# Performance work log

Hardware: AMD Instinct MI355X
Metric: run time of the kernel (lower is better)

## Reference

```python
import jax, jax.numpy as jnp
import numpy as np

B, N, M, C, K = 2, 8192, 4096, 64, 16
HID = 256
EPS_BN = 1e-5


def setup_inputs() -> dict:
    key = jax.random.key(0)
    ks = jax.random.split(key, 16)
    def rn(i, shape, scale=1.0):
        return jax.random.normal(ks[i], shape, jnp.float32) * scale
    return {
        "pcl": rn(0, (B, M, 3)),
        "pcl_noise": rn(1, (B, N, 3)),
        "feature": rn(2, (B, M, C)),
        # MLP_CONV (2d 1x1): 6 -> 256 (BN+ReLU) -> C
        "w2a": rn(3, (HID, 6), 0.3), "b2a": rn(4, (HID,), 0.1),
        "g2a": 1.0 + rn(5, (HID,), 0.1), "bt2a": rn(6, (HID,), 0.1),
        "w2b": rn(7, (C, HID), 0.1), "b2b": rn(8, (C,), 0.1),
        # MLP_CONV_1d: 3C -> C (BN+ReLU) -> C
        "w1a": rn(9, (C, 3 * C), 0.1), "b1a": rn(10, (C,), 0.1),
        "g1a": 1.0 + rn(11, (C,), 0.1), "bt1a": rn(12, (C,), 0.1),
        "w1b": rn(13, (C, C), 0.1), "b1b": rn(14, (C,), 0.1),
    }


def _sqdist(x, y):  # [B,n,3],[B,m,3] -> [B,n,m]
    return (jnp.sum(x * x, -1, keepdims=True)
            - 2.0 * jnp.einsum('bnc,bmc->bnm', x, y)
            + jnp.sum(y * y, -1)[:, None, :])


def _gather(x, idx):  # x [B,M,D], idx [B,...] -> [B,...,D]
    return jax.vmap(lambda xb, ib: xb[ib])(x, idx)


def _bn(h, g, b):  # inference BatchNorm: running mean 0, var 1
    return h * (g / jnp.sqrt(1.0 + EPS_BN)) + b


def reference(pcl, pcl_noise, feature, w2a, b2a, g2a, bt2a, w2b, b2b,
              w1a, b1a, g1a, bt1a, w1b, b1b):
    # nearest clean point for each noisy point (knn_points K=1)
    close_idx = jnp.argmin(_sqdist(pcl_noise, pcl), axis=-1)          # [B,N]
    close_point = _gather(pcl, close_idx)                             # [B,N,3]
    # K nearest neighbors of close_point within pcl (dil_knn, d=1)
    _, idx = jax.lax.top_k(-_sqdist(close_point, pcl), K)             # [B,N,K]
    knn_points = _gather(pcl, idx)[:, :, 1:, :]                       # [B,N,K-1,3]
    knn_feat = _gather(feature, idx)[:, :, 1:, :]                     # [B,N,K-1,C]
    close_feat = _gather(feature, close_idx)                          # [B,N,C]

    delta = knn_points - pcl_noise[:, :, None, :]                     # [B,N,K-1,3]
    dst = jnp.linalg.norm(delta, axis=-1)                             # [B,N,K-1]
    e = jnp.exp(-10.0 * dst)
    weight = e / (jnp.sum(e, -1, keepdims=True) + 1e-7)               # [B,N,K-1]

    cp = jnp.broadcast_to(close_point[:, :, None, :], delta.shape)
    delta_points = jnp.concatenate([delta, cp], axis=-1)              # [B,N,K-1,6]

    # MLP_CONV2 (1x1 convs over channel dim)
    h = jnp.einsum('bnkc,oc->bnko', delta_points, w2a) + b2a
    h = jax.nn.relu(_bn(h, g2a, bt2a))
    pf = jnp.einsum('bnkc,oc->bnko', h, w2b) + b2b                    # [B,N,K-1,C]

    point_feature = jnp.einsum('bnk,bnkc->bnc', weight, pf)           # [B,N,C]
    co_feature = jnp.einsum('bnk,bnkc->bnc', weight, knn_feat)        # [B,N,C]
    df = jnp.concatenate([close_feat, co_feature, point_feature], -1)  # [B,N,3C]

    # MLP_CONV_1d
    h1 = jnp.einsum('bnc,oc->bno', df, w1a) + b1a
    h1 = jax.nn.relu(_bn(h1, g1a, bt1a))
    return jnp.einsum('bnc,oc->bno', h1, w1b) + b1b                   # [B,N,C]
```

## Files before the change

### kernel.cpp

```cpp
#include <hip/hip_runtime.h>
#include <float.h>

typedef unsigned short u16;
typedef unsigned int u32;
typedef unsigned char u8;

typedef float f32x4 __attribute__((ext_vector_type(4)));
typedef short bh8   __attribute__((ext_vector_type(8)));

__device__ __forceinline__ float bf(u16 u) { return __uint_as_float(((u32)u) << 16); }
__device__ __forceinline__ u16 f2bf(float v) {
    u32 x = __float_as_uint(v);
    u32 r = x + 0x7fffu + ((x >> 16) & 1u);
    return (u16)(r >> 16);
}
__device__ __forceinline__ int detect_f32(const void* probe) {
    const u16* u = (const u16*)probe;
    u16 v = u[(threadIdx.x & 63) * 2];
    int e = (int)((v >> 7) & 0xFF);
    int moderate = (e >= 100) && (e <= 140);
    return __popcll(__ballot(moderate)) < 48;
}
__device__ __forceinline__ float ldv(int f32, const void* p, int i) {
    return f32 ? ((const float*)p)[i] : bf(((const u16*)p)[i]);
}
__device__ __forceinline__ float dot3(float x0, float x1, float x2,
                                      float y0, float y1, float y2) {
    return __fmaf_rn(x2, y2, __fmaf_rn(x1, y1, __fmul_rn(x0, y0)));
}
__device__ __forceinline__ u32 mkey32(float d) {
    u32 f = __float_as_uint(d);
    return f ^ (u32)((((int)f) >> 31) | 0x80000000);
}
__device__ __forceinline__ bh8 ldb(const void* p) { return *(const bh8*)p; }
__device__ __forceinline__ f32x4 mfma16(bh8 a, bh8 b, f32x4 c) {
    return __builtin_amdgcn_mfma_f32_16x16x32_bf16(a, b, c, 0, 0, 0);
}

__global__ __launch_bounds__(256) void k_pre(const void* __restrict__ probe,
                                             const void* __restrict__ w2b,
                                             const void* __restrict__ w1a,
                                             const void* __restrict__ w1b,
                                             u32* __restrict__ canonb,
                                             const void* __restrict__ pcl,
                                             float4* __restrict__ pcl4) {
    int f32 = detect_f32(probe);
    int bx = blockIdx.x, t = threadIdx.x;
    if (bx < 64) {
        int ix = bx * 256 + t;
        const void* src; int j;
        if (ix < 8192)       { src = w2b; j = ix; }
        else if (ix < 14336) { src = w1a; j = ix - 8192; }
        else                 { src = w1b; j = ix - 14336; }
        u32 out;
        if (f32) {
            const float* f = (const float*)src;
            out = ((u32)f2bf(f[2*j+1]) << 16) | (u32)f2bf(f[2*j]);
        } else {
            const u16* su = (const u16*)src;
            out = ((u32)su[2*j+1] << 16) | (u32)su[2*j];
        }
        canonb[ix] = out;
    } else {
        int i = (bx - 64) * 256 + t;
        float x = ldv(f32, pcl, i*3+0), y = ldv(f32, pcl, i*3+1), z = ldv(f32, pcl, i*3+2);
        float s = __fadd_rn(__fadd_rn(__fmul_rn(x,x), __fmul_rn(y,y)), __fmul_rn(z,z));
        pcl4[i] = make_float4(x, y, z, s);
    }
}

__global__ __launch_bounds__(256) void k_sel(const float4* __restrict__ pcl4,
                                             const void* __restrict__ noise,
                                             u16* __restrict__ cidx,
                                             u16* __restrict__ knn) {
    __shared__ __align__(16) char arena[16384];
    int bx = blockIdx.x;
    int r9 = bx % 9, c9 = bx / 9;
    int t = threadIdx.x, lane = t & 63, wv = t >> 6;

    if (r9 == 0) {
        float4* tile = (float4*)arena;
        int f32 = detect_f32(noise);
        int g = t >> 4, s = t & 15;
        int q = c9 * 16 + g;
        int b = q >> 13;
        const float4* src = pcl4 + ((size_t)b << 12);
        float x0 = ldv(f32, noise, q*3+0), x1 = ldv(f32, noise, q*3+1), x2 = ldv(f32, noise, q*3+2);
        float sx = __fadd_rn(__fadd_rn(__fmul_rn(x0,x0), __fmul_rn(x1,x1)), __fmul_rn(x2,x2));
        float bd = FLT_MAX; int bi = 0;
        for (int ch = 0; ch < 4; ++ch) {
            __syncthreads();
#pragma unroll
            for (int i = 0; i < 4; ++i) { int ix = t + (i << 8); tile[ix] = src[(ch << 10) + ix]; }
            __syncthreads();
            for (int j = 0; j < 64; ++j) {
                int cl = (j << 4) + s;
                float4 p = tile[cl];
                float dot = dot3(x0, x1, x2, p.x, p.y, p.z);
                float d = __fadd_rn(__fsub_rn(sx, __fmul_rn(2.0f, dot)), p.w);
                int c = (ch << 10) + cl;
                if (d < bd) { bd = d; bi = c; }
            }
        }
#pragma unroll
        for (int m = 8; m >= 1; m >>= 1) {
            float od = __shfl_xor(bd, m);
            int   oi = __shfl_xor(bi, m);
            if (od < bd || (od == bd && oi < bi)) { bd = od; bi = oi; }
        }
        if (s == 0) cidx[q] = (u16)(bi & 4095);
        return;
    }

    u8*  bins = (u8*)arena;
    u32* hist = (u32*)(arena + 4096);
    u32* skey = (u32*)(arena + 5120);
    u16* sidx = (u16*)(arena + 6144);
    float* rmn = (float*)(arena + 6656);
    float* rmx = (float*)(arena + 6672);
    u32* scnt = (u32*)(arena + 6688);
    int* ibst = (int*)(arena + 6692);

    int q = c9 * 8 + (r9 - 1);
    int b = q >> 12;
    const float4* src = pcl4 + ((size_t)b << 12);
    float4 Q = src[q & 4095];
    float x0 = Q.x, x1 = Q.y, x2 = Q.z, sx = Q.w;
    hist[t] = 0;
    if (t == 0) *scnt = 0;
    {
        float4 p = src[t << 4];
        float dot = dot3(x0, x1, x2, p.x, p.y, p.z);
        float d = __fadd_rn(__fsub_rn(sx, __fmul_rn(2.0f, dot)), p.w);
        float mn = d, mx = d;
#pragma unroll
        for (int m = 32; m >= 1; m >>= 1) {
            mn = fminf(mn, __shfl_xor(mn, m));
            mx = fmaxf(mx, __shfl_xor(mx, m));
        }
        if (lane == 0) { rmn[wv] = mn; rmx[wv] = mx; }
    }
    __syncthreads();
    float dmn = fminf(fminf(rmn[0], rmn[1]), fminf(rmn[2], rmn[3]));
    float dmx = fmaxf(fmaxf(rmx[0], rmx[1]), fmaxf(rmx[2], rmx[3]));
    float sc = 1024.0f / fmaxf(dmx - dmn, 1e-20f);
#pragma unroll 4
    for (int j = 0; j < 16; ++j) {
        int cin = (j << 8) + t;
        float4 p = src[cin];
        float dot = dot3(x0, x1, x2, p.x, p.y, p.z);
        float d = __fadd_rn(__fsub_rn(sx, __fmul_rn(2.0f, dot)), p.w);
        float fb = fminf(fmaxf((d - dmn) * sc, 0.0f), 255.0f);
        int bn = (int)fb;
        bins[cin] = (u8)bn;
        if (bn < 255) atomicAdd(&hist[bn], 1u);
    }
    __syncthreads();
    if (t < 64) {
        u32 c0 = hist[4*lane], c1 = hist[4*lane+1];
        u32 c2 = hist[4*lane+2], c3 = hist[4*lane+3];
        u32 loc = c0 + c1 + c2 + c3;
        u32 x = loc;
#pragma unroll
        for (int off = 1; off < 64; off <<= 1) { u32 v = __shfl_up(x, off); if (lane >= off) x += v; }
        u32 excl = x - loc;
        int cand = 999;
        if (excl + c0 >= 16u) cand = 4*lane;
        else if (excl + c0 + c1 >= 16u) cand = 4*lane + 1;
        else if (excl + c0 + c1 + c2 >= 16u) cand = 4*lane + 2;
        else if (excl + loc >= 16u) cand = 4*lane + 3;
#pragma unroll
        for (int m = 32; m >= 1; m >>= 1) cand = min(cand, __shfl_xor(cand, m));
        if (lane == 0) *ibst = cand;
    }
    __syncthreads();
    int bstar = *ibst;
#pragma unroll
    for (int j = 0; j < 16; ++j) {
        int cin = (j << 8) + t;
        if ((int)bins[cin] <= bstar) {
            u32 pos = atomicAdd(scnt, 1u);
            if (pos < 256u) {
                float4 p = src[cin];
                float dot = dot3(x0, x1, x2, p.x, p.y, p.z);
                float d = __fadd_rn(__fsub_rn(sx, __fmul_rn(2.0f, dot)), p.w);
                skey[pos] = mkey32(d);
                sidx[pos] = (u16)cin;
            }
        }
    }
    __syncthreads();
    u32 n = *scnt;
    if (n <= 256u) {
        for (u32 e = (u32)t; e < n; e += 256u) {
            u32 k = skey[e]; u32 i = (u32)sidx[e];
            int rank = 0;
            for (u32 j = 0; j < n; ++j) {
                u32 kj = skey[j]; u32 ij = (u32)sidx[j];
                rank += (kj < k) || (kj == k && ij < i);
            }
            if (rank < 16) knn[((size_t)q << 4) + rank] = (u16)i;
        }
    } else if (t < 64) {
        u32 k0=~0u,k1=~0u,k2=~0u,k3=~0u,k4=~0u,k5=~0u,k6=~0u,k7=~0u,
            k8=~0u,k9=~0u,k10=~0u,k11=~0u,k12=~0u,k13=~0u,k14=~0u,k15=~0u;
        u32 i0r=0,i1r=0,i2r=0,i3r=0,i4r=0,i5r=0,i6r=0,i7r=0,
            i8r=0,i9r=0,i10r=0,i11r=0,i12r=0,i13r=0,i14r=0,i15r=0;
        for (int j = 0; j < 64; ++j) {
            int cin = (j << 6) + lane;
            float4 p = src[cin];
            float dot = dot3(x0, x1, x2, p.x, p.y, p.z);
            float d = __fadd_rn(__fsub_rn(sx, __fmul_rn(2.0f, dot)), p.w);
            u32 v = mkey32(d); u32 vi = (u32)cin;
            if (v < k15) {
                { u32 c_=(v<k0); u32 nk=c_?v:k0; u32 nv=c_?k0:v; u32 ni=c_?vi:i0r; u32 nj=c_?i0r:vi; k0=nk;i0r=ni;v=nv;vi=nj; }
                { u32 c_=(v<k1); u32 nk=c_?v:k1; u32 nv=c_?k1:v; u32 ni=c_?vi:i1r; u32 nj=c_?i1r:vi; k1=nk;i1r=ni;v=nv;vi=nj; }
                { u32 c_=(v<k2); u32 nk=c_?v:k2; u32 nv=c_?k2:v; u32 ni=c_?vi:i2r; u32 nj=c_?i2r:vi; k2=nk;i2r=ni;v=nv;vi=nj; }
                { u32 c_=(v<k3); u32 nk=c_?v:k3; u32 nv=c_?k3:v; u32 ni=c_?vi:i3r; u32 nj=c_?i3r:vi; k3=nk;i3r=ni;v=nv;vi=nj; }
                { u32 c_=(v<k4); u32 nk=c_?v:k4; u32 nv=c_?k4:v; u32 ni=c_?vi:i4r; u32 nj=c_?i4r:vi; k4=nk;i4r=ni;v=nv;vi=nj; }
                { u32 c_=(v<k5); u32 nk=c_?v:k5; u32 nv=c_?k5:v; u32 ni=c_?vi:i5r; u32 nj=c_?i5r:vi; k5=nk;i5r=ni;v=nv;vi=nj; }
                { u32 c_=(v<k6); u32 nk=c_?v:k6; u32 nv=c_?k6:v; u32 ni=c_?vi:i6r; u32 nj=c_?i6r:vi; k6=nk;i6r=ni;v=nv;vi=nj; }
                { u32 c_=(v<k7); u32 nk=c_?v:k7; u32 nv=c_?k7:v; u32 ni=c_?vi:i7r; u32 nj=c_?i7r:vi; k7=nk;i7r=ni;v=nv;vi=nj; }
                { u32 c_=(v<k8); u32 nk=c_?v:k8; u32 nv=c_?k8:v; u32 ni=c_?vi:i8r; u32 nj=c_?i8r:vi; k8=nk;i8r=ni;v=nv;vi=nj; }
                { u32 c_=(v<k9); u32 nk=c_?v:k9; u32 nv=c_?k9:v; u32 ni=c_?vi:i9r; u32 nj=c_?i9r:vi; k9=nk;i9r=ni;v=nv;vi=nj; }
                { u32 c_=(v<k10); u32 nk=c_?v:k10; u32 nv=c_?k10:v; u32 ni=c_?vi:i10r; u32 nj=c_?i10r:vi; k10=nk;i10r=ni;v=nv;vi=nj; }
                { u32 c_=(v<k11); u32 nk=c_?v:k11; u32 nv=c_?k11:v; u32 ni=c_?vi:i11r; u32 nj=c_?i11r:vi; k11=nk;i11r=ni;v=nv;vi=nj; }
                { u32 c_=(v<k12); u32 nk=c_?v:k12; u32 nv=c_?k12:v; u32 ni=c_?vi:i12r; u32 nj=c_?i12r:vi; k12=nk;i12r=ni;v=nv;vi=nj; }
                { u32 c_=(v<k13); u32 nk=c_?v:k13; u32 nv=c_?k13:v; u32 ni=c_?vi:i13r; u32 nj=c_?i13r:vi; k13=nk;i13r=ni;v=nv;vi=nj; }
                { u32 c_=(v<k14); u32 nk=c_?v:k14; u32 nv=c_?k14:v; u32 ni=c_?vi:i14r; u32 nj=c_?i14r:vi; k14=nk;i14r=ni;v=nv;vi=nj; }
                { u32 c_=(v<k15); u32 nk=c_?v:k15; u32 nv=c_?k15:v; u32 ni=c_?vi:i15r; u32 nj=c_?i15r:vi; k15=nk;i15r=ni;v=nv;vi=nj; }
            }
        }
        u32 myres = 0;
        for (int o = 0; o < 16; ++o) {
            u32 bk = k0, bi2 = i0r;
#pragma unroll
            for (int m = 32; m >= 1; m >>= 1) {
                u32 ok = __shfl_xor(bk, m), oi = __shfl_xor(bi2, m);
                if (ok < bk || (ok == bk && oi < bi2)) { bk = ok; bi2 = oi; }
            }
            if (lane == o) myres = bi2;
            if (k0 == bk && i0r == bi2) {
                k0=k1; i0r=i1r; k1=k2; i1r=i2r; k2=k3; i2r=i3r; k3=k4; i3r=i4r;
                k4=k5; i4r=i5r; k5=k6; i5r=i6r; k6=k7; i6r=i7r; k7=k8; i7r=i8r;
                k8=k9; i8r=i9r; k9=k10; i9r=i10r; k10=k11; i10r=i11r; k11=k12; i11r=i12r;
                k12=k13; i12r=i13r; k13=k14; i13r=i14r; k14=k15; i14r=i15r;
                k15=~0u; i15r=0xFFFFu;
            }
        }
        if (lane < 16) knn[((size_t)q << 4) + lane] = (u16)myres;
    }
}

__global__ __launch_bounds__(256) void k_tail(const float4* __restrict__ pcl4,
                                              const void* __restrict__ noise,
                                              const void* __restrict__ feat,
                                              const u16* __restrict__ cidx,
                                              const u16* __restrict__ knn,
                                              const void* __restrict__ w2a,
                                              const void* __restrict__ b2a,
                                              const void* __restrict__ g2a,
                                              const void* __restrict__ bt2a,
                                              const u32* __restrict__ canonb,
                                              const void* __restrict__ b2b,
                                              const void* __restrict__ b1a,
                                              const void* __restrict__ g1a,
                                              const void* __restrict__ bt1a,
                                              const void* __restrict__ b1b,
                                              void* __restrict__ outp) {
    __shared__ __align__(16) char arena[39744];
    char* dpb_hi = arena;
    char* dpb_lo = arena + 4352;
    char* wbt    = arena + 8704;
    char* wsbp   = arena + 9984;
    u16*  jbuf   = (u16*)(arena + 10048);
    char* hbm_   = arena + 10560;
    char* dfm    = arena + 27200;
    char* h1m    = arena;

    int f32 = detect_f32(noise);
    int t = threadIdx.x, lane = t & 63, wv = t >> 6;
    int g = lane >> 4, l15 = lane & 15;
    int qbb = blockIdx.x * 16;
    int o_lane = wv * 16 + l15;
    const float rbn = 1.0f / sqrtf(1.0f + 1e-5f);
    const char* cb = (const char*)canonb;
    const f32x4 zero4 = {0.f, 0.f, 0.f, 0.f};

    float of2r[4];
    bh8 wH[4];
#pragma unroll
    for (int j = 0; j < 4; ++j) {
        int oh = wv*64 + j*16 + l15;
        float sc = ldv(f32, g2a, oh) * rbn;
        of2r[j] = ldv(f32, b2a, oh) * sc + ldv(f32, bt2a, oh);
        bh8 wz = (bh8){0,0,0,0,0,0,0,0};
        if (g < 3) {
#pragma unroll
            for (int c = 0; c < 6; ++c) {
                float wval = ldv(f32, w2a, oh*6 + c) * sc;
                u16 h = f2bf(wval);
                u16 e = (g == 2) ? f2bf(wval - bf(h)) : h;
                wz[c] = (short)e;
            }
        }
        wH[j] = wz;
    }
    float s1o  = ldv(f32, g1a, o_lane) * rbn;
    float o1o  = ldv(f32, b1a, o_lane) * s1o + ldv(f32, bt1a, o_lane);
    float b2bo = ldv(f32, b2b, o_lane);
    float b1fo = ldv(f32, b1b, o_lane);

    {
        int s = lane & 15;
        int ql = wv*4 + (lane >> 4);
        int q = qbb + ql;
        int pbase = (q >> 13) << 12;
        int ci = ((int)cidx[q]) & 4095;
        float4 cp = pcl4[pbase + ci];
        float x0 = ldv(f32, noise, q*3+0), x1 = ldv(f32, noise, q*3+1), x2 = ldv(f32, noise, q*3+2);
        float e = 0.0f;
        if (s >= 1) {
            int jk = ((int)knn[(size_t)(pbase + ci) * 16 + s]) & 4095;
            float4 p = pcl4[pbase + jk];
            float d0 = p.x - x0, d1 = p.y - x1, d2 = p.z - x2;
            float dst = sqrtf(__fadd_rn(__fadd_rn(__fmul_rn(d0,d0), __fmul_rn(d1,d1)), __fmul_rn(d2,d2)));
            e = expf(-10.0f * dst);
            float v6[6] = {d0, d1, d2, cp.x, cp.y, cp.z};
            bh8 HW = (bh8){0,0,0,0,0,0,0,0};
            bh8 LW = (bh8){0,0,0,0,0,0,0,0};
#pragma unroll
            for (int c = 0; c < 6; ++c) {
                u16 hh = f2bf(v6[c]);
                u16 ll = f2bf(v6[c] - bf(hh));
                HW[c] = (short)hh;
                LW[c] = (short)ll;
            }
            *(bh8*)(dpb_hi + (ql*17 + s)*16) = HW;
            *(bh8*)(dpb_lo + (ql*17 + s)*16) = LW;
            jbuf[ql*16 + s] = (u16)jk;
        }
        float es = e;
#pragma unroll
        for (int m = 8; m >= 1; m >>= 1) es += __shfl_xor(es, m, 16);
        float den = es + 1e-7f;
        if (s >= 1) *(float*)(wbt + s*80 + ql*4) = e / den;
        if (s == 0) *(float*)(wsbp + ql*4) = es / den;
    }
    __syncthreads();

#pragma unroll
    for (int qq = 0; qq < 4; ++qq) {
        int qloc = wv*4 + qq;
        int q = qbb + qloc;
        int pbase = (q >> 13) << 12;
        int ci = ((int)cidx[q]) & 4095;
        size_t fcb = ((size_t)(pbase + ci)) << 6;
        float c0, c1 = 0.0f;
        if (f32) {
            const float* ff = (const float*)feat;
            c0 = ff[fcb + lane];
#pragma unroll
            for (int k = 1; k < 16; ++k) {
                float wk = *(const float*)(wbt + k*80 + qloc*4);
                c1 += wk * ff[(((size_t)(pbase + (int)jbuf[qloc*16 + k])) << 6) + lane];
            }
        } else {
            const u16* fb = (const u16*)feat;
            c0 = bf(fb[fcb + lane]);
#pragma unroll
            for (int k = 1; k < 16; ++k) {
                float wk = *(const float*)(wbt + k*80 + qloc*4);
                c1 += wk * bf(fb[(((size_t)(pbase + (int)jbuf[qloc*16 + k])) << 6) + lane]);
            }
        }
        char* dr = dfm + qloc*784;
        u16 h0 = f2bf(c0); u16 l0 = f2bf(c0 - bf(h0));
        u16 h1v = f2bf(c1); u16 l1v = f2bf(c1 - bf(h1v));
        *(u16*)(dr + (size_t)lane*2)         = h0;
        *(u16*)(dr + (size_t)(192+lane)*2)   = l0;
        *(u16*)(dr + (size_t)(64+lane)*2)    = h1v;
        *(u16*)(dr + (size_t)(256+lane)*2)   = l1v;
    }

    {
        f32x4 hba[4];
#pragma unroll
        for (int j = 0; j < 4; ++j) hba[j] = zero4;
#pragma unroll 2
        for (int k = 1; k < 16; ++k) {
            bh8 af;
            if (g < 3) {
                const char* base = (g == 1) ? dpb_lo : dpb_hi;
                af = ldb(base + (l15*17 + k)*16);
            } else {
                af = (bh8){0,0,0,0,0,0,0,0};
            }
            f32x4 wk4 = *(const f32x4*)(wbt + k*80 + g*16);
#pragma unroll
            for (int j = 0; j < 4; ++j) {
                f32x4 d = mfma16(af, wH[j], zero4);
#pragma unroll
                for (int r = 0; r < 4; ++r)
                    hba[j][r] += wk4[r] * fmaxf(d[r] + of2r[j], 0.0f);
            }
        }
#pragma unroll
        for (int j = 0; j < 4; ++j)
#pragma unroll
            for (int r = 0; r < 4; ++r) {
                int q = g*4 + r;
                int o = wv*64 + j*16 + l15;
                float x = hba[j][r];
                u16 h = f2bf(x); u16 l = f2bf(x - bf(h));
                *(u16*)(hbm_ + q*1040 + (size_t)o*2)       = h;
                *(u16*)(hbm_ + q*1040 + 512 + (size_t)o*2) = l;
            }
    }
    __syncthreads();

    {
        f32x4 acA = zero4, acB = zero4;
#pragma unroll 2
        for (int ks = 0; ks < 8; ++ks) {
            bh8 bw = ldb(cb + (size_t)o_lane*512 + ks*64 + g*16);
            bh8 aH = ldb(hbm_ + l15*1040 + ks*64 + g*16);
            bh8 aL = ldb(hbm_ + l15*1040 + 512 + ks*64 + g*16);
            acA = mfma16(aH, bw, acA);
            acB = mfma16(aL, bw, acB);
        }
        f32x4 wsb4 = *(const f32x4*)(wsbp + g*16);
#pragma unroll
        for (int r = 0; r < 4; ++r) {
            int q = g*4 + r;
            float pf = acA[r] + acB[r] + b2bo * wsb4[r];
            u16 h = f2bf(pf); u16 l = f2bf(pf - bf(h));
            *(u16*)(dfm + q*784 + (size_t)(128 + o_lane)*2) = h;
            *(u16*)(dfm + q*784 + (size_t)(320 + o_lane)*2) = l;
        }
    }
    __syncthreads();

    {
        f32x4 acA = zero4, acB = zero4;
#pragma unroll 2
        for (int ks = 0; ks < 6; ++ks) {
            bh8 bw = ldb(cb + 32768 + (size_t)o_lane*384 + ks*64 + g*16);
            bh8 aH = ldb(dfm + l15*784 + ks*64 + g*16);
            bh8 aL = ldb(dfm + l15*784 + 384 + ks*64 + g*16);
            acA = mfma16(aH, bw, acA);
            acB = mfma16(aL, bw, acB);
        }
#pragma unroll
        for (int r = 0; r < 4; ++r) {
            int q = g*4 + r;
            float z = (acA[r] + acB[r]) * s1o + o1o;
            z = fmaxf(z, 0.0f);
            u16 h = f2bf(z); u16 l = f2bf(z - bf(h));
            *(u16*)(h1m + q*272 + (size_t)o_lane*2)       = h;
            *(u16*)(h1m + q*272 + 128 + (size_t)o_lane*2) = l;
        }
    }
    __syncthreads();

    {
        bh8 bw0 = ldb(cb + 57344 + (size_t)o_lane*128 + g*16);
        bh8 bw1 = ldb(cb + 57344 + (size_t)o_lane*128 + 64 + g*16);
        f32x4 ac = zero4;
        { bh8 a = ldb(h1m + l15*272 +   0 + g*16); ac = mfma16(a, bw0, ac); }
        { bh8 a = ldb(h1m + l15*272 +  64 + g*16); ac = mfma16(a, bw1, ac); }
        { bh8 a = ldb(h1m + l15*272 + 128 + g*16); ac = mfma16(a, bw0, ac); }
        { bh8 a = ldb(h1m + l15*272 + 192 + g*16); ac = mfma16(a, bw1, ac); }
#pragma unroll
        for (int r = 0; r < 4; ++r) {
            int q = g*4 + r;
            float ov = ac[r] + b1fo;
            size_t ob = ((size_t)(qbb + q) << 6) + o_lane;
            if (f32) ((float*)outp)[ob] = ov;
            else     ((u16*)outp)[ob]   = f2bf(ov);
        }
    }
}

extern "C" void kernel_launch(void* const* d_in, const int* in_sizes, int n_in,
                              void* d_out, int out_size, void* d_ws, size_t ws_size,
                              hipStream_t stream) {
    const void* pcl   = d_in[0];
    const void* noise = d_in[1];
    const void* feat  = d_in[2];
    const void* w2a   = d_in[3];
    const void* b2a   = d_in[4];
    const void* g2a   = d_in[5];
    const void* bt2a  = d_in[6];
    const void* w2b   = d_in[7];
    const void* b2b   = d_in[8];
    const void* w1a   = d_in[9];
    const void* b1a   = d_in[10];
    const void* g1a   = d_in[11];
    const void* bt1a  = d_in[12];
    const void* w1b   = d_in[13];
    const void* b1b   = d_in[14];

    char* ws = (char*)d_ws;
    float4* pcl4 = (float4*)ws;
    u16* cidx = (u16*)(ws + 131072);
    u16* knn  = (u16*)(ws + 163840);
    u32* canonb = (u32*)(ws + 425984);

    k_pre  <<<96,   256, 0, stream>>>(noise, w2b, w1a, w1b, canonb, pcl, pcl4);
    k_sel  <<<9216, 256, 0, stream>>>(pcl4, noise, cidx, knn);
    k_tail <<<1024, 256, 0, stream>>>(pcl4, noise, feat, cidx, knn,
                                      w2a, b2a, g2a, bt2a, canonb, b2b,
                                      b1a, g1a, bt1a, b1b, d_out);
}
```

Baseline: 213.3 us.

## Process two kNN queries per block in k_sel to share point-cloud loads

```diff
diff --git a/kernel.cpp b/kernel.cpp
--- a/kernel.cpp
+++ b/kernel.cpp
@@ -28,6 +28,10 @@
                                       float y0, float y1, float y2) {
     return __fmaf_rn(x2, y2, __fmaf_rn(x1, y1, __fmul_rn(x0, y0)));
 }
+__device__ __forceinline__ float qdist(float x0, float x1, float x2, float sx, float4 p) {
+    float dot = dot3(x0, x1, x2, p.x, p.y, p.z);
+    return __fadd_rn(__fsub_rn(sx, __fmul_rn(2.0f, dot)), p.w);
+}
 __device__ __forceinline__ u32 mkey32(float d) {
     u32 f = __float_as_uint(d);
     return f ^ (u32)((((int)f) >> 31) | 0x80000000);
@@ -35,6 +39,56 @@
 __device__ __forceinline__ bh8 ldb(const void* p) { return *(const bh8*)p; }
 __device__ __forceinline__ f32x4 mfma16(bh8 a, bh8 b, f32x4 c) {
     return __builtin_amdgcn_mfma_f32_16x16x32_bf16(a, b, c, 0, 0, 0);
+}
+
+__device__ __forceinline__ void knn_fallback(const float4* __restrict__ src,
+                                             float x0, float x1, float x2, float sx,
+                                             int q, u16* __restrict__ knn, int lane) {
+    u32 k0=~0u,k1=~0u,k2=~0u,k3=~0u,k4=~0u,k5=~0u,k6=~0u,k7=~0u,
+        k8=~0u,k9=~0u,k10=~0u,k11=~0u,k12=~0u,k13=~0u,k14=~0u,k15=~0u;
+    u32 i0r=0,i1r=0,i2r=0,i3r=0,i4r=0,i5r=0,i6r=0,i7r=0,
+        i8r=0,i9r=0,i10r=0,i11r=0,i12r=0,i13r=0,i14r=0,i15r=0;
+    for (int j = 0; j < 64; ++j) {
+        int cin = (j << 6) + lane;
+        float d = qdist(x0, x1, x2, sx, src[cin]);
+        u32 v = mkey32(d); u32 vi = (u32)cin;
+        if (v < k15) {
+            { u32 c_=(v<k0); u32 nk=c_?v:k0; u32 nv=c_?k0:v; u32 ni=c_?vi:i0r; u32 nj=c_?i0r:vi; k0=nk;i0r=ni;v=nv;vi=nj; }
+            { u32 c_=(v<k1); u32 nk=c_?v:k1; u32 nv=c_?k1:v; u32 ni=c_?vi:i1r; u32 nj=c_?i1r:vi; k1=nk;i1r=ni;v=nv;vi=nj; }
+            { u32 c_=(v<k2); u32 nk=c_?v:k2; u32 nv=c_?k2:v; u32 ni=c_?vi:i2r; u32 nj=c_?i2r:vi; k2=nk;i2r=ni;v=nv;vi=nj; }
+            { u32 c_=(v<k3); u32 nk=c_?v:k3; u32 nv=c_?k3:v; u32 ni=c_?vi:i3r; u32 nj=c_?i3r:vi; k3=nk;i3r=ni;v=nv;vi=nj; }
+            { u32 c_=(v<k4); u32 nk=c_?v:k4; u32 nv=c_?k4:v; u32 ni=c_?vi:i4r; u32 nj=c_?i4r:vi; k4=nk;i4r=ni;v=nv;vi=nj; }
+            { u32 c_=(v<k5); u32 nk=c_?v:k5; u32 nv=c_?k5:v; u32 ni=c_?vi:i5r; u32 nj=c_?i5r:vi; k5=nk;i5r=ni;v=nv;vi=nj; }
+            { u32 c_=(v<k6); u32 nk=c_?v:k6; u32 nv=c_?k6:v; u32 ni=c_?vi:i6r; u32 nj=c_?i6r:vi; k6=nk;i6r=ni;v=nv;vi=nj; }
+            { u32 c_=(v<k7); u32 nk=c_?v:k7; u32 nv=c_?k7:v; u32 ni=c_?vi:i7r; u32 nj=c_?i7r:vi; k7=nk;i7r=ni;v=nv;vi=nj; }
+            { u32 c_=(v<k8); u32 nk=c_?v:k8; u32 nv=c_?k8:v; u32 ni=c_?vi:i8r; u32 nj=c_?i8r:vi; k8=nk;i8r=ni;v=nv;vi=nj; }
+            { u32 c_=(v<k9); u32 nk=c_?v:k9; u32 nv=c_?k9:v; u32 ni=c_?vi:i9r; u32 nj=c_?i9r:vi; k9=nk;i9r=ni;v=nv;vi=nj; }
+            { u32 c_=(v<k10); u32 nk=c_?v:k10; u32 nv=c_?k10:v; u32 ni=c_?vi:i10r; u32 nj=c_?i10r:vi; k10=nk;i10r=ni;v=nv;vi=nj; }
+            { u32 c_=(v<k11); u32 nk=c_?v:k11; u32 nv=c_?k11:v; u32 ni=c_?vi:i11r; u32 nj=c_?i11r:vi; k11=nk;i11r=ni;v=nv;vi=nj; }
+            { u32 c_=(v<k12); u32 nk=c_?v:k12; u32 nv=c_?k12:v; u32 ni=c_?vi:i12r; u32 nj=c_?i12r:vi; k12=nk;i12r=ni;v=nv;vi=nj; }
+            { u32 c_=(v<k13); u32 nk=c_?v:k13; u32 nv=c_?k13:v; u32 ni=c_?vi:i13r; u32 nj=c_?i13r:vi; k13=nk;i13r=ni;v=nv;vi=nj; }
+            { u32 c_=(v<k14); u32 nk=c_?v:k14; u32 nv=c_?k14:v; u32 ni=c_?vi:i14r; u32 nj=c_?i14r:vi; k14=nk;i14r=ni;v=nv;vi=nj; }
+            { u32 c_=(v<k15); u32 nk=c_?v:k15; u32 nv=c_?k15:v; u32 ni=c_?vi:i15r; u32 nj=c_?i15r:vi; k15=nk;i15r=ni;v=nv;vi=nj; }
+        }
+    }
+    u32 myres = 0;
+    for (int o = 0; o < 16; ++o) {
+        u32 bk = k0, bi2 = i0r;
+#pragma unroll
+        for (int m = 32; m >= 1; m >>= 1) {
+            u32 ok = __shfl_xor(bk, m), oi = __shfl_xor(bi2, m);
+            if (ok < bk || (ok == bk && oi < bi2)) { bk = ok; bi2 = oi; }
+        }
+        if (lane == o) myres = bi2;
+        if (k0 == bk && i0r == bi2) {
+            k0=k1; i0r=i1r; k1=k2; i1r=i2r; k2=k3; i2r=i3r; k3=k4; i3r=i4r;
+            k4=k5; i4r=i5r; k5=k6; i5r=i6r; k6=k7; i6r=i7r; k7=k8; i7r=i8r;
+            k8=k9; i8r=i9r; k9=k10; i9r=i10r; k10=k11; i10r=i11r; k11=k12; i11r=i12r;
+            k12=k13; i12r=i13r; k13=k14; i13r=i14r; k14=k15; i14r=i15r;
+            k15=~0u; i15r=0xFFFFu;
+        }
+    }
+    if (lane < 16) knn[((size_t)q << 4) + lane] = (u16)myres;
 }
 
 __global__ __launch_bounds__(256) void k_pre(const void* __restrict__ probe,
@@ -73,32 +127,31 @@
                                              const void* __restrict__ noise,
                                              u16* __restrict__ cidx,
                                              u16* __restrict__ knn) {
-    __shared__ __align__(16) char arena[16384];
+    __shared__ __align__(16) char arena[32768];
     int bx = blockIdx.x;
-    int r9 = bx % 9, c9 = bx / 9;
+    int r5 = bx % 5, c5 = bx / 5;
     int t = threadIdx.x, lane = t & 63, wv = t >> 6;
 
-    if (r9 == 0) {
+    if (r5 == 0) {
         float4* tile = (float4*)arena;
         int f32 = detect_f32(noise);
         int g = t >> 4, s = t & 15;
-        int q = c9 * 16 + g;
+        int q = c5 * 16 + g;
         int b = q >> 13;
         const float4* src = pcl4 + ((size_t)b << 12);
         float x0 = ldv(f32, noise, q*3+0), x1 = ldv(f32, noise, q*3+1), x2 = ldv(f32, noise, q*3+2);
         float sx = __fadd_rn(__fadd_rn(__fmul_rn(x0,x0), __fmul_rn(x1,x1)), __fmul_rn(x2,x2));
         float bd = FLT_MAX; int bi = 0;
-        for (int ch = 0; ch < 4; ++ch) {
+        for (int ch = 0; ch < 2; ++ch) {
             __syncthreads();
 #pragma unroll
-            for (int i = 0; i < 4; ++i) { int ix = t + (i << 8); tile[ix] = src[(ch << 10) + ix]; }
+            for (int i = 0; i < 8; ++i) { int ix = t + (i << 8); tile[ix] = src[(ch << 11) + ix]; }
             __syncthreads();
-            for (int j = 0; j < 64; ++j) {
+            for (int j = 0; j < 128; ++j) {
                 int cl = (j << 4) + s;
                 float4 p = tile[cl];
-                float dot = dot3(x0, x1, x2, p.x, p.y, p.z);
-                float d = __fadd_rn(__fsub_rn(sx, __fmul_rn(2.0f, dot)), p.w);
-                int c = (ch << 10) + cl;
+                float d = qdist(x0, x1, x2, sx, p);
+                int c = (ch << 11) + cl;
                 if (d < bd) { bd = d; bi = c; }
             }
         }
@@ -112,53 +165,72 @@
         return;
     }
 
-    u8*  bins = (u8*)arena;
-    u32* hist = (u32*)(arena + 4096);
-    u32* skey = (u32*)(arena + 5120);
-    u16* sidx = (u16*)(arena + 6144);
-    float* rmn = (float*)(arena + 6656);
-    float* rmx = (float*)(arena + 6672);
-    u32* scnt = (u32*)(arena + 6688);
-    int* ibst = (int*)(arena + 6692);
-
-    int q = c9 * 8 + (r9 - 1);
-    int b = q >> 12;
+    u8*  bins0 = (u8*)arena;
+    u8*  bins1 = (u8*)(arena + 4096);
+    u32* hist0 = (u32*)(arena + 8192);
+    u32* hist1 = (u32*)(arena + 9216);
+    u32* skey0 = (u32*)(arena + 10240);
+    u32* skey1 = (u32*)(arena + 11264);
+    u16* sidx0 = (u16*)(arena + 12288);
+    u16* sidx1 = (u16*)(arena + 12800);
+    float* rmn0 = (float*)(arena + 13312);
+    float* rmx0 = (float*)(arena + 13328);
+    float* rmn1 = (float*)(arena + 13344);
+    float* rmx1 = (float*)(arena + 13360);
+    u32* scnt0 = (u32*)(arena + 13376);
+    u32* scnt1 = (u32*)(arena + 13380);
+    int* ibst0 = (int*)(arena + 13384);
+    int* ibst1 = (int*)(arena + 13388);
+
+    int qp = c5 * 4 + (r5 - 1);
+    int q0 = qp << 1, q1 = q0 | 1;
+    int b = q0 >> 12;
     const float4* src = pcl4 + ((size_t)b << 12);
-    float4 Q = src[q & 4095];
-    float x0 = Q.x, x1 = Q.y, x2 = Q.z, sx = Q.w;
-    hist[t] = 0;
-    if (t == 0) *scnt = 0;
+    float4 Q0 = src[q0 & 4095];
+    float4 Q1 = src[q1 & 4095];
+    float ax0 = Q0.x, ax1 = Q0.y, ax2 = Q0.z, asx = Q0.w;
+    float bx0 = Q1.x, bx1 = Q1.y, bx2 = Q1.z, bsx = Q1.w;
+    hist0[t] = 0; hist1[t] = 0;
+    if (t == 0) { *scnt0 = 0; *scnt1 = 0; }
     {
         float4 p = src[t << 4];
-        float dot = dot3(x0, x1, x2, p.x, p.y, p.z);
-        float d = __fadd_rn(__fsub_rn(sx, __fmul_rn(2.0f, dot)), p.w);
-        float mn = d, mx = d;
+        float da = qdist(ax0, ax1, ax2, asx, p);
+        float db = qdist(bx0, bx1, bx2, bsx, p);
+        float mn0 = da, mx0 = da, mn1 = db, mx1 = db;
 #pragma unroll
         for (int m = 32; m >= 1; m >>= 1) {
-            mn = fminf(mn, __shfl_xor(mn, m));
-            mx = fmaxf(mx, __shfl_xor(mx, m));
-        }
-        if (lane == 0) { rmn[wv] = mn; rmx[wv] = mx; }
-    }
-    __syncthreads();
-    float dmn = fminf(fminf(rmn[0], rmn[1]), fminf(rmn[2], rmn[3]));
-    float dmx = fmaxf(fmaxf(rmx[0], rmx[1]), fmaxf(rmx[2], rmx[3]));
-    float sc = 1024.0f / fmaxf(dmx - dmn, 1e-20f);
+            mn0 = fminf(mn0, __shfl_xor(mn0, m));
+            mx0 = fmaxf(mx0, __shfl_xor(mx0, m));
+            mn1 = fminf(mn1, __shfl_xor(mn1, m));
+            mx1 = fmaxf(mx1, __shfl_xor(mx1, m));
+        }
+        if (lane == 0) { rmn0[wv] = mn0; rmx0[wv] = mx0; rmn1[wv] = mn1; rmx1[wv] = mx1; }
+    }
+    __syncthreads();
+    float dmn0 = fminf(fminf(rmn0[0], rmn0[1]), fminf(rmn0[2], rmn0[3]));
+    float dmx0 = fmaxf(fmaxf(rmx0[0], rmx0[1]), fmaxf(rmx0[2], rmx0[3]));
+    float sc0f = 1024.0f / fmaxf(dmx0 - dmn0, 1e-20f);
+    float dmn1 = fminf(fminf(rmn1[0], rmn1[1]), fminf(rmn1[2], rmn1[3]));
+    float dmx1 = fmaxf(fmaxf(rmx1[0], rmx1[1]), fmaxf(rmx1[2], rmx1[3]));
+    float sc1f = 1024.0f / fmaxf(dmx1 - dmn1, 1e-20f);
 #pragma unroll 4
     for (int j = 0; j < 16; ++j) {
         int cin = (j << 8) + t;
         float4 p = src[cin];
-        float dot = dot3(x0, x1, x2, p.x, p.y, p.z);
-        float d = __fadd_rn(__fsub_rn(sx, __fmul_rn(2.0f, dot)), p.w);
-        float fb = fminf(fmaxf((d - dmn) * sc, 0.0f), 255.0f);
-        int bn = (int)fb;
-        bins[cin] = (u8)bn;
-        if (bn < 255) atomicAdd(&hist[bn], 1u);
-    }
-    __syncthreads();
-    if (t < 64) {
-        u32 c0 = hist[4*lane], c1 = hist[4*lane+1];
-        u32 c2 = hist[4*lane+2], c3 = hist[4*lane+3];
+        float d0 = qdist(ax0, ax1, ax2, asx, p);
+        float d1 = qdist(bx0, bx1, bx2, bsx, p);
+        int bn0 = (int)fminf(fmaxf((d0 - dmn0) * sc0f, 0.0f), 255.0f);
+        int bn1 = (int)fminf(fmaxf((d1 - dmn1) * sc1f, 0.0f), 255.0f);
+        bins0[cin] = (u8)bn0;
+        bins1[cin] = (u8)bn1;
+        if (bn0 < 255) atomicAdd(&hist0[bn0], 1u);
+        if (bn1 < 255) atomicAdd(&hist1[bn1], 1u);
+    }
+    __syncthreads();
+    if (wv < 2) {
+        u32* hh = wv ? hist1 : hist0;
+        u32 c0 = hh[4*lane], c1 = hh[4*lane+1];
+        u32 c2 = hh[4*lane+2], c3 = hh[4*lane+3];
         u32 loc = c0 + c1 + c2 + c3;
         u32 x = loc;
 #pragma unroll
@@ -171,84 +243,63 @@
         else if (excl + loc >= 16u) cand = 4*lane + 3;
 #pragma unroll
         for (int m = 32; m >= 1; m >>= 1) cand = min(cand, __shfl_xor(cand, m));
-        if (lane == 0) *ibst = cand;
-    }
-    __syncthreads();
-    int bstar = *ibst;
+        if (lane == 0) { if (wv) *ibst1 = cand; else *ibst0 = cand; }
+    }
+    __syncthreads();
+    int bstar0 = *ibst0, bstar1 = *ibst1;
 #pragma unroll
     for (int j = 0; j < 16; ++j) {
         int cin = (j << 8) + t;
-        if ((int)bins[cin] <= bstar) {
-            u32 pos = atomicAdd(scnt, 1u);
-            if (pos < 256u) {
-                float4 p = src[cin];
-                float dot = dot3(x0, x1, x2, p.x, p.y, p.z);
-                float d = __fadd_rn(__fsub_rn(sx, __fmul_rn(2.0f, dot)), p.w);
-                skey[pos] = mkey32(d);
-                sidx[pos] = (u16)cin;
-            }
-        }
-    }
-    __syncthreads();
-    u32 n = *scnt;
-    if (n <= 256u) {
-        for (u32 e = (u32)t; e < n; e += 256u) {
-            u32 k = skey[e]; u32 i = (u32)sidx[e];
-            int rank = 0;
-            for (u32 j = 0; j < n; ++j) {
-                u32 kj = skey[j]; u32 ij = (u32)sidx[j];
-                rank += (kj < k) || (kj == k && ij < i);
-            }
-            if (rank < 16) knn[((size_t)q << 4) + rank] = (u16)i;
-        }
-    } else if (t < 64) {
-        u32 k0=~0u,k1=~0u,k2=~0u,k3=~0u,k4=~0u,k5=~0u,k6=~0u,k7=~0u,
-            k8=~0u,k9=~0u,k10=~0u,k11=~0u,k12=~0u,k13=~0u,k14=~0u,k15=~0u;
-        u32 i0r=0,i1r=0,i2r=0,i3r=0,i4r=0,i5r=0,i6r=0,i7r=0,
-            i8r=0,i9r=0,i10r=0,i11r=0,i12r=0,i13r=0,i14r=0,i15r=0;
-        for (int j = 0; j < 64; ++j) {
-            int cin = (j << 6) + lane;
+        int s0 = (int)bins0[cin] <= bstar0;
+        int s1 = (int)bins1[cin] <= bstar1;
+        if (s0 | s1) {
             float4 p = src[cin];
-            float dot = dot3(x0, x1, x2, p.x, p.y, p.z);
-            float d = __fadd_rn(__fsub_rn(sx, __fmul_rn(2.0f, dot)), p.w);
-            u32 v = mkey32(d); u32 vi = (u32)cin;
-            if (v < k15) {
-                { u32 c_=(v<k0); u32 nk=c_?v:k0; u32 nv=c_?k0:v; u32 ni=c_?vi:i0r; u32 nj=c_?i0r:vi; k0=nk;i0r=ni;v=nv;vi=nj; }
-                { u32 c_=(v<k1); u32 nk=c_?v:k1; u32 nv=c_?k1:v; u32 ni=c_?vi:i1r; u32 nj=c_?i1r:vi; k1=nk;i1r=ni;v=nv;vi=nj; }
-                { u32 c_=(v<k2); u32 nk=c_?v:k2; u32 nv=c_?k2:v; u32 ni=c_?vi:i2r; u32 nj=c_?i2r:vi; k2=nk;i2r=ni;v=nv;vi=nj; }
-                { u32 c_=(v<k3); u32 nk=c_?v:k3; u32 nv=c_?k3:v; u32 ni=c_?vi:i3r; u32 nj=c_?i3r:vi; k3=nk;i3r=ni;v=nv;vi=nj; }
-                { u32 c_=(v<k4); u32 nk=c_?v:k4; u32 nv=c_?k4:v; u32 ni=c_?vi:i4r; u32 nj=c_?i4r:vi; k4=nk;i4r=ni;v=nv;vi=nj; }
-                { u32 c_=(v<k5); u32 nk=c_?v:k5; u32 nv=c_?k5:v; u32 ni=c_?vi:i5r; u32 nj=c_?i5r:vi; k5=nk;i5r=ni;v=nv;vi=nj; }
-                { u32 c_=(v<k6); u32 nk=c_?v:k6; u32 nv=c_?k6:v; u32 ni=c_?vi:i6r; u32 nj=c_?i6r:vi; k6=nk;i6r=ni;v=nv;vi=nj; }
-                { u32 c_=(v<k7); u32 nk=c_?v:k7; u32 nv=c_?k7:v; u32 ni=c_?vi:i7r; u32 nj=c_?i7r:vi; k7=nk;i7r=ni;v=nv;vi=nj; }
-                { u32 c_=(v<k8); u32 nk=c_?v:k8; u32 nv=c_?k8:v; u32 ni=c_?vi:i8r; u32 nj=c_?i8r:vi; k8=nk;i8r=ni;v=nv;vi=nj; }
-                { u32 c_=(v<k9); u32 nk=c_?v:k9; u32 nv=c_?k9:v; u32 ni=c_?vi:i9r; u32 nj=c_?i9r:vi; k9=nk;i9r=ni;v=nv;vi=nj; }
-                { u32 c_=(v<k10); u32 nk=c_?v:k10; u32 nv=c_?k10:v; u32 ni=c_?vi:i10r; u32 nj=c_?i10r:vi; k10=nk;i10r=ni;v=nv;vi=nj; }
-                { u32 c_=(v<k11); u32 nk=c_?v:k11; u32 nv=c_?k11:v; u32 ni=c_?vi:i11r; u32 nj=c_?i11r:vi; k11=nk;i11r=ni;v=nv;vi=nj; }
-                { u32 c_=(v<k12); u32 nk=c_?v:k12; u32 nv=c_?k12:v; u32 ni=c_?vi:i12r; u32 nj=c_?i12r:vi; k12=nk;i12r=ni;v=nv;vi=nj; }
-                { u32 c_=(v<k13); u32 nk=c_?v:k13; u32 nv=c_?k13:v; u32 ni=c_?vi:i13r; u32 nj=c_?i13r:vi; k13=nk;i13r=ni;v=nv;vi=nj; }
-                { u32 c_=(v<k14); u32 nk=c_?v:k14; u32 nv=c_?k14:v; u32 ni=c_?vi:i14r; u32 nj=c_?i14r:vi; k14=nk;i14r=ni;v=nv;vi=nj; }
-                { u32 c_=(v<k15); u32 nk=c_?v:k15; u32 nv=c_?k15:v; u32 ni=c_?vi:i15r; u32 nj=c_?i15r:vi; k15=nk;i15r=ni;v=nv;vi=nj; }
-            }
-        }
-        u32 myres = 0;
-        for (int o = 0; o < 16; ++o) {
-            u32 bk = k0, bi2 = i0r;
-#pragma unroll
-            for (int m = 32; m >= 1; m >>= 1) {
-                u32 ok = __shfl_xor(bk, m), oi = __shfl_xor(bi2, m);
-                if (ok < bk || (ok == bk && oi < bi2)) { bk = ok; bi2 = oi; }
-            }
-            if (lane == o) myres = bi2;
-            if (k0 == bk && i0r == bi2) {
-                k0=k1; i0r=i1r; k1=k2; i1r=i2r; k2=k3; i2r=i3r; k3=k4; i3r=i4r;
-                k4=k5; i4r=i5r; k5=k6; i5r=i6r; k6=k7; i6r=i7r; k7=k8; i7r=i8r;
-                k8=k9; i8r=i9r; k9=k10; i9r=i10r; k10=k11; i10r=i11r; k11=k12; i11r=i12r;
-                k12=k13; i12r=i13r; k13=k14; i13r=i14r; k14=k15; i14r=i15r;
-                k15=~0u; i15r=0xFFFFu;
-            }
-        }
-        if (lane < 16) knn[((size_t)q << 4) + lane] = (u16)myres;
+            if (s0) {
+                u32 pos = atomicAdd(scnt0, 1u);
+                if (pos < 256u) {
+                    float d = qdist(ax0, ax1, ax2, asx, p);
+                    skey0[pos] = mkey32(d); sidx0[pos] = (u16)cin;
+                }
+            }
+            if (s1) {
+                u32 pos = atomicAdd(scnt1, 1u);
+                if (pos < 256u) {
+                    float d = qdist(bx0, bx1, bx2, bsx, p);
+                    skey1[pos] = mkey32(d); sidx1[pos] = (u16)cin;
+                }
+            }
+        }
+    }
+    __syncthreads();
+    u32 n0 = *scnt0, n1 = *scnt1;
+    if (t < 128) {
+        if (n0 <= 256u) {
+            for (u32 e = (u32)t; e < n0; e += 128u) {
+                u32 k = skey0[e]; u32 i = (u32)sidx0[e];
+                int rank = 0;
+                for (u32 j = 0; j < n0; ++j) {
+                    u32 kj = skey0[j]; u32 ij = (u32)sidx0[j];
+                    rank += (kj < k) || (kj == k && ij < i);
+                }
+                if (rank < 16) knn[((size_t)q0 << 4) + rank] = (u16)i;
+            }
+        } else if (wv == 0) {
+            knn_fallback(src, ax0, ax1, ax2, asx, q0, knn, lane);
+        }
+    } else {
+        if (n1 <= 256u) {
+            for (u32 e = (u32)(t - 128); e < n1; e += 128u) {
+                u32 k = skey1[e]; u32 i = (u32)sidx1[e];
+                int rank = 0;
+                for (u32 j = 0; j < n1; ++j) {
+                    u32 kj = skey1[j]; u32 ij = (u32)sidx1[j];
+                    rank += (kj < k) || (kj == k && ij < i);
+                }
+                if (rank < 16) knn[((size_t)q1 << 4) + rank] = (u16)i;
+            }
+        } else if (wv == 2) {
+            knn_fallback(src, bx0, bx1, bx2, bsx, q1, knn, lane);
+        }
     }
 }
 
@@ -508,7 +559,7 @@
     u32* canonb = (u32*)(ws + 425984);
 
     k_pre  <<<96,   256, 0, stream>>>(noise, w2b, w1a, w1b, canonb, pcl, pcl4);
-    k_sel  <<<9216, 256, 0, stream>>>(pcl4, noise, cidx, knn);
+    k_sel  <<<5120, 256, 0, stream>>>(pcl4, noise, cidx, knn);
     k_tail <<<1024, 256, 0, stream>>>(pcl4, noise, feat, cidx, knn,
                                       w2a, b2a, g2a, bt2a, canonb, b2b,
                                       b1a, g1a, bt1a, b1b, d_out);
```

New measurement: 205.6 us. 3.6% less time.
